# Kernel optimization log

Measured on AMD Instinct MI355X. Metric: run time of the kernel, lower is better.

Reference implementation:

```python
import jax, jax.numpy as jnp
import numpy as np

N = 8192
DIN = 256
DOUT = 128
ALPHA = 0.2      # leaky-relu negative slope
K_MAX = 32       # static upper bound on action.max()+1 (action in [0, 32))
NEG_BIG = -9.0e15


def setup_inputs() -> dict:
    key = jax.random.key(0)
    ks = jax.random.split(key, 6)
    xavier_w = 1.414 * np.sqrt(6.0 / (DIN + DOUT))
    xavier_a = 1.414 * np.sqrt(6.0 / (DOUT + 1))
    return {
        "input": jax.random.normal(ks[0], (N, DIN), dtype=jnp.float32),
        "adj": jax.random.randint(ks[1], (N, N), 0, 2, dtype=jnp.int32),
        "action": jax.random.randint(ks[2], (N,), 0, K_MAX, dtype=jnp.int32),
        "W": jax.random.uniform(ks[3], (DIN, DOUT), jnp.float32, -xavier_w, xavier_w),
        "a_self": jax.random.uniform(ks[4], (DOUT, 1), jnp.float32, -xavier_a, xavier_a),
        "a_neighs": jax.random.uniform(ks[5], (DOUT, 1), jnp.float32, -xavier_a, xavier_a),
        "breadth_policy": 1,
    }


def reference(input, adj, action, W, a_self, a_neighs, breadth_policy):
    h = input @ W                                  # [N, DOUT]
    attn_self = h @ a_self                         # [N, 1]
    attn_neighs = h @ a_neighs                     # [N, 1]
    e = jax.nn.leaky_relu(attn_self + attn_neighs.T, negative_slope=ALPHA)  # [N, N]
    masked = jnp.where(adj > 0, e, jnp.float32(NEG_BIG))
    attention = jax.nn.softmax(masked, axis=1)     # [N, N]
    if breadth_policy:
        # static K_MAX >= action.max()+1; thresholds only read index action[i]
        top_vals, _ = jax.lax.top_k(attention, K_MAX)          # [N, K_MAX], sorted desc
        thresholds = top_vals[jnp.arange(N), action]           # [N]
        attention = jnp.where(attention < thresholds[:, None], 0.0, attention)
    h_prime = attention @ h                        # [N, DOUT]
    return jax.nn.elu(h_prime)                     # concat=True
```

## Files before the change

kernel.cpp:

```cpp
#include <hip/hip_runtime.h>
#include <cstdint>
#include <cstddef>

#define NN   8192
#define DIN  256
#define DOUT 128
#define LRA  0.2f

__global__ __launch_bounds__(256) void gemm_h_kernel(
    const float* __restrict__ input, const float* __restrict__ W,
    float* __restrict__ h)
{
    __shared__ float tile[16][DIN];
    const int row0 = blockIdx.x * 16;
    {
        const float4* in4 = (const float4*)(input + (size_t)row0 * DIN);
        float4* t4 = (float4*)&tile[0][0];
        for (int k = threadIdx.x; k < 16 * DIN / 4; k += 256) t4[k] = in4[k];
    }
    __syncthreads();
    const int c = threadIdx.x & 127;
    const int g = threadIdx.x >> 7;
    float acc[8] = {0.f, 0.f, 0.f, 0.f, 0.f, 0.f, 0.f, 0.f};
    for (int k = 0; k < DIN; k += 4) {
        const float w0 = W[(k + 0) * DOUT + c];
        const float w1 = W[(k + 1) * DOUT + c];
        const float w2 = W[(k + 2) * DOUT + c];
        const float w3 = W[(k + 3) * DOUT + c];
        #pragma unroll
        for (int m = 0; m < 8; ++m) {
            const float4 av = *(const float4*)&tile[g * 8 + m][k];
            acc[m] += av.x * w0 + av.y * w1 + av.z * w2 + av.w * w3;
        }
    }
    #pragma unroll
    for (int m = 0; m < 8; ++m)
        h[(size_t)(row0 + g * 8 + m) * DOUT + c] = acc[m];
}

__global__ __launch_bounds__(256) void attn_vec_kernel(
    const float* __restrict__ h, const float* __restrict__ a_self,
    const float* __restrict__ a_neighs, float* __restrict__ s,
    float* __restrict__ t)
{
    const int wid  = (blockIdx.x * 256 + threadIdx.x) >> 6;
    const int lane = threadIdx.x & 63;
    if (wid >= NN) return;
    const float h0 = h[(size_t)wid * DOUT + lane];
    const float h1 = h[(size_t)wid * DOUT + 64 + lane];
    float vs = h0 * a_self[lane]   + h1 * a_self[64 + lane];
    float vn = h0 * a_neighs[lane] + h1 * a_neighs[64 + lane];
    for (int off = 32; off > 0; off >>= 1) {
        vs += __shfl_down(vs, off);
        vn += __shfl_down(vn, off);
    }
    if (lane == 0) { s[wid] = vs; t[wid] = vn; }
}

__global__ __launch_bounds__(256) void rank_kernel(
    const float* __restrict__ t, int* __restrict__ order)
{
    __shared__ float tl[NN];
    __shared__ int   part[8][32];
    for (int k = threadIdx.x; k < NN; k += 256) tl[k] = t[k];
    __syncthreads();
    const int jloc = threadIdx.x & 31;
    const int seg  = threadIdx.x >> 5;
    const int j    = blockIdx.x * 32 + jloc;
    const float tj = tl[j];
    int r = 0;
    const int k0 = seg * (NN / 8);
    for (int k = k0; k < k0 + NN / 8; ++k) {
        const float tk = tl[k];
        r += (tk > tj) ? 1 : ((tk == tj && k < j) ? 1 : 0);
    }
    part[seg][jloc] = r;
    __syncthreads();
    if (threadIdx.x < 32) {
        int rr = 0;
        #pragma unroll
        for (int ss = 0; ss < 8; ++ss) rr += part[ss][threadIdx.x];
        order[rr] = blockIdx.x * 32 + threadIdx.x;
    }
}

__global__ __launch_bounds__(256) void gat_row_kernel(
    const int* __restrict__ adj, const float* __restrict__ s_arr,
    const float* __restrict__ t_arr, const int* __restrict__ order,
    const int* __restrict__ action, const float* __restrict__ h,
    const int* __restrict__ policy, float* __restrict__ out)
{
    __shared__ float tl[NN];
    __shared__ float red[256];
    __shared__ float numlds[2][128];
    __shared__ int   sel_j[64];
    __shared__ float sel_w[64];
    __shared__ int   sel_cnt_sh;
    __shared__ int   done_sh;

    const int row = blockIdx.x;
    const int tid = threadIdx.x;
    {
        const float4* t4 = (const float4*)t_arr;
        float4* tl4 = (float4*)tl;
        for (int k = tid; k < NN / 4; k += 256) tl4[k] = t4[k];
    }
    __syncthreads();

    const float s    = s_arr[row];
    const float tmax = tl[order[0]];
    const float zc   = s + tmax;
    const float C    = fmaxf(zc, LRA * zc);

    const int4*   arow = (const int4*)(adj + (size_t)row * NN);
    const float4* tl4c = (const float4*)tl;
    float acc = 0.f;
    #pragma unroll
    for (int k = 0; k < 8; ++k) {
        const int idx = tid + k * 256;
        const int4   a  = arow[idx];
        const float4 tv = tl4c[idx];
        float z, e, w;
        z = s + tv.x; e = fmaxf(z, LRA * z); w = __expf(e - C); if (a.x > 0) acc += w;
        z = s + tv.y; e = fmaxf(z, LRA * z); w = __expf(e - C); if (a.y > 0) acc += w;
        z = s + tv.z; e = fmaxf(z, LRA * z); w = __expf(e - C); if (a.z > 0) acc += w;
        z = s + tv.w; e = fmaxf(z, LRA * z); w = __expf(e - C); if (a.w > 0) acc += w;
    }
    red[tid] = acc;
    __syncthreads();
    for (int off = 128; off > 0; off >>= 1) {
        if (tid < off) red[tid] += red[tid + off];
        __syncthreads();
    }
    const float l = red[0];

    int K = action[row] + 1;
    if (policy[0] == 0) K = 0x7FFFFFFF;
    const int c = tid & 127;
    const int g = tid >> 7;
    float accv = 0.f;

    const int lane = tid & 63;
    float tthr = -3.0e38f;
    int found = 0;
    int cnt = 0;
    int base = 0;

    while (true) {
        if (tid < 64) {
            const int p = base + lane;
            int j = 0, valid = 0;
            float tj = -3.0e38f;
            if (p < NN) {
                j     = order[p];
                tj    = tl[j];
                valid = (adj[(size_t)row * NN + j] > 0) ? 1 : 0;
            }
            const unsigned long long vm = __ballot(valid);
            if (!found) {
                const int cv = __popcll(vm);
                if (cnt + cv >= K) {
                    const int need = K - cnt;
                    const int myrank =
                        __popcll(vm & ((1ull << lane) - 1ull)) + 1;
                    const unsigned long long pm =
                        __ballot(valid && (myrank == need));
                    const int L = __ffsll((long long)pm) - 1;
                    tthr  = __shfl(tj, L);
                    found = 1;
                } else {
                    cnt += cv;
                }
            }
            const int selected = valid && (tj >= tthr);
            const unsigned long long sm = __ballot(selected);
            const int pos = __popcll(sm & ((1ull << lane) - 1ull));
            if (selected) {
                const float z = s + tj;
                const float e = fmaxf(z, LRA * z);
                sel_j[pos] = j;
                sel_w[pos] = __expf(e - C);
            }
            if (lane == 0) {
                sel_cnt_sh = __popcll(sm);
                const int nb = base + 64;
                int dn;
                if (nb >= NN)      dn = 1;
                else if (found)    dn = (tl[order[nb]] < tthr) ? 1 : 0;
                else               dn = 0;
                done_sh = dn;
            }
        }
        __syncthreads();
        const int nsel = sel_cnt_sh;
        const int dn   = done_sh;
        for (int e2 = g; e2 < nsel; e2 += 2)
            accv += sel_w[e2] * h[(size_t)sel_j[e2] * DOUT + c];
        base += 64;
        if (dn) break;
        __syncthreads();
    }

    numlds[g][c] = accv;
    __syncthreads();
    if (tid < 128) {
        const float v = (numlds[0][tid] + numlds[1][tid]) / l;
        out[(size_t)row * DOUT + tid] = (v > 0.f) ? v : expm1f(v);
    }
}

extern "C" void kernel_launch(void* const* d_in, const int* in_sizes, int n_in,
                              void* d_out, int out_size, void* d_ws,
                              size_t ws_size, hipStream_t stream)
{
    const float* input    = (const float*)d_in[0];
    const int*   adj      = (const int*)d_in[1];
    const int*   action   = (const int*)d_in[2];
    const float* W        = (const float*)d_in[3];
    const float* a_self   = (const float*)d_in[4];
    const float* a_neighs = (const float*)d_in[5];
    const int*   policy   = (const int*)d_in[6];
    float* out = (float*)d_out;

    float* ws    = (float*)d_ws;
    float* h     = ws;
    float* s     = ws + (size_t)NN * DOUT;
    float* t     = s + NN;
    int*   order = (int*)(t + NN);

    hipLaunchKernelGGL(gemm_h_kernel, dim3(512), dim3(256), 0, stream,
                       input, W, h);
    hipLaunchKernelGGL(attn_vec_kernel, dim3(2048), dim3(256), 0, stream,
                       h, a_self, a_neighs, s, t);
    hipLaunchKernelGGL(rank_kernel, dim3(256), dim3(256), 0, stream,
                       t, order);
    hipLaunchKernelGGL(gat_row_kernel, dim3(8192), dim3(256), 0, stream,
                       adj, s, t, order, action, h, policy, out);
}
```

Before: 429.8 us.

## Fuse all GAT stages into one cooperative persistent kernel with grid syncs

Replaces the four kernel launches (projection GEMM, attention vectors, ranking, per-row softmax/top-k aggregation) with one cooperative kernel of 512 blocks. Each block handles 16 rows end to end and uses grid.sync between phases. The attention-vector dot products are now computed straight from the GEMM accumulators. Ranking is redistributed so each block ranks its own 16 rows. The aim is to remove launch gaps and the reloads of t into LDS. The cost is only 512 blocks for the bandwidth-heavy adjacency phase (down from 8192), with each block looping over 16 rows serially, which may reduce latency hiding.

```diff
diff --git a/kernel.cpp b/kernel.cpp
--- a/kernel.cpp
+++ b/kernel.cpp
@@ -1,211 +1,227 @@
 #include <hip/hip_runtime.h>
+#include <hip/hip_cooperative_groups.h>
 #include <cstdint>
 #include <cstddef>
 
-#define NN   8192
-#define DIN  256
-#define DOUT 128
-#define LRA  0.2f
-
-__global__ __launch_bounds__(256) void gemm_h_kernel(
-    const float* __restrict__ input, const float* __restrict__ W,
-    float* __restrict__ h)
+namespace cg = cooperative_groups;
+
+#define NN    8192
+#define DIN   256
+#define DOUT  128
+#define LRA   0.2f
+#define RPB   16
+#define NB    512
+
+__global__ __launch_bounds__(256, 2) void gat_fused_kernel(
+    const float* __restrict__ input, const int* __restrict__ adj,
+    const int* __restrict__ action, const float* __restrict__ W,
+    const float* __restrict__ a_self, const float* __restrict__ a_neighs,
+    const int* __restrict__ policy, float* __restrict__ out,
+    float* __restrict__ h, float* __restrict__ s_arr,
+    float* __restrict__ t_arr, int* __restrict__ order)
 {
-    __shared__ float tile[16][DIN];
-    const int row0 = blockIdx.x * 16;
-    {
-        const float4* in4 = (const float4*)(input + (size_t)row0 * DIN);
-        float4* t4 = (float4*)&tile[0][0];
-        for (int k = threadIdx.x; k < 16 * DIN / 4; k += 256) t4[k] = in4[k];
-    }
-    __syncthreads();
-    const int c = threadIdx.x & 127;
-    const int g = threadIdx.x >> 7;
-    float acc[8] = {0.f, 0.f, 0.f, 0.f, 0.f, 0.f, 0.f, 0.f};
-    for (int k = 0; k < DIN; k += 4) {
-        const float w0 = W[(k + 0) * DOUT + c];
-        const float w1 = W[(k + 1) * DOUT + c];
-        const float w2 = W[(k + 2) * DOUT + c];
-        const float w3 = W[(k + 3) * DOUT + c];
-        #pragma unroll
-        for (int m = 0; m < 8; ++m) {
-            const float4 av = *(const float4*)&tile[g * 8 + m][k];
-            acc[m] += av.x * w0 + av.y * w1 + av.z * w2 + av.w * w3;
-        }
-    }
-    #pragma unroll
-    for (int m = 0; m < 8; ++m)
-        h[(size_t)(row0 + g * 8 + m) * DOUT + c] = acc[m];
-}
-
-__global__ __launch_bounds__(256) void attn_vec_kernel(
-    const float* __restrict__ h, const float* __restrict__ a_self,
-    const float* __restrict__ a_neighs, float* __restrict__ s,
-    float* __restrict__ t)
-{
-    const int wid  = (blockIdx.x * 256 + threadIdx.x) >> 6;
-    const int lane = threadIdx.x & 63;
-    if (wid >= NN) return;
-    const float h0 = h[(size_t)wid * DOUT + lane];
-    const float h1 = h[(size_t)wid * DOUT + 64 + lane];
-    float vs = h0 * a_self[lane]   + h1 * a_self[64 + lane];
-    float vn = h0 * a_neighs[lane] + h1 * a_neighs[64 + lane];
-    for (int off = 32; off > 0; off >>= 1) {
-        vs += __shfl_down(vs, off);
-        vn += __shfl_down(vn, off);
-    }
-    if (lane == 0) { s[wid] = vs; t[wid] = vn; }
-}
-
-__global__ __launch_bounds__(256) void rank_kernel(
-    const float* __restrict__ t, int* __restrict__ order)
-{
-    __shared__ float tl[NN];
-    __shared__ int   part[8][32];
-    for (int k = threadIdx.x; k < NN; k += 256) tl[k] = t[k];
-    __syncthreads();
-    const int jloc = threadIdx.x & 31;
-    const int seg  = threadIdx.x >> 5;
-    const int j    = blockIdx.x * 32 + jloc;
-    const float tj = tl[j];
-    int r = 0;
-    const int k0 = seg * (NN / 8);
-    for (int k = k0; k < k0 + NN / 8; ++k) {
-        const float tk = tl[k];
-        r += (tk > tj) ? 1 : ((tk == tj && k < j) ? 1 : 0);
-    }
-    part[seg][jloc] = r;
-    __syncthreads();
-    if (threadIdx.x < 32) {
-        int rr = 0;
-        #pragma unroll
-        for (int ss = 0; ss < 8; ++ss) rr += part[ss][threadIdx.x];
-        order[rr] = blockIdx.x * 32 + threadIdx.x;
-    }
-}
-
-__global__ __launch_bounds__(256) void gat_row_kernel(
-    const int* __restrict__ adj, const float* __restrict__ s_arr,
-    const float* __restrict__ t_arr, const int* __restrict__ order,
-    const int* __restrict__ action, const float* __restrict__ h,
-    const int* __restrict__ policy, float* __restrict__ out)
-{
-    __shared__ float tl[NN];
-    __shared__ float red[256];
-    __shared__ float numlds[2][128];
+    cg::grid_group grid = cg::this_grid();
+
+    __shared__ union {
+        float tile[RPB][DIN];
+        float tl[NN];
+    } u;
+    __shared__ float red[4];
+    __shared__ float numlds[2][DOUT];
+    __shared__ float pr[4][16];
+    __shared__ int   prank[4][RPB];
     __shared__ int   sel_j[64];
     __shared__ float sel_w[64];
     __shared__ int   sel_cnt_sh;
     __shared__ int   done_sh;
 
-    const int row = blockIdx.x;
-    const int tid = threadIdx.x;
+    const int tid  = threadIdx.x;
+    const int row0 = blockIdx.x * RPB;
+    const int c    = tid & 127;
+    const int g    = tid >> 7;
+    const int lane = tid & 63;
+    const int wave = tid >> 6;
+
+    {
+        const float4* in4 = (const float4*)(input + (size_t)row0 * DIN);
+        float4* t4 = (float4*)&u.tile[0][0];
+        #pragma unroll
+        for (int k = 0; k < 4; ++k) t4[tid + k * 256] = in4[tid + k * 256];
+    }
+    __syncthreads();
+    {
+        float acc[8];
+        #pragma unroll
+        for (int m = 0; m < 8; ++m) acc[m] = 0.f;
+        for (int k = 0; k < DIN; k += 4) {
+            const float w0 = W[(k + 0) * DOUT + c];
+            const float w1 = W[(k + 1) * DOUT + c];
+            const float w2 = W[(k + 2) * DOUT + c];
+            const float w3 = W[(k + 3) * DOUT + c];
+            #pragma unroll
+            for (int m = 0; m < 8; ++m) {
+                const float4 av = *(const float4*)&u.tile[g * 8 + m][k];
+                acc[m] += av.x * w0 + av.y * w1 + av.z * w2 + av.w * w3;
+            }
+        }
+        #pragma unroll
+        for (int m = 0; m < 8; ++m)
+            h[(size_t)(row0 + g * 8 + m) * DOUT + c] = acc[m];
+
+        const float as = a_self[c];
+        const float an = a_neighs[c];
+        #pragma unroll
+        for (int m = 0; m < 8; ++m) {
+            float vs = acc[m] * as;
+            float vt = acc[m] * an;
+            for (int off = 32; off > 0; off >>= 1) {
+                vs += __shfl_down(vs, off);
+                vt += __shfl_down(vt, off);
+            }
+            if (lane == 0) { pr[wave][2 * m] = vs; pr[wave][2 * m + 1] = vt; }
+        }
+    }
+    __syncthreads();
+    if (tid < 16) {
+        const int m  = tid & 7;
+        const int gg = tid >> 3;
+        const int r  = row0 + gg * 8 + m;
+        s_arr[r] = pr[2 * gg][2 * m]     + pr[2 * gg + 1][2 * m];
+        t_arr[r] = pr[2 * gg][2 * m + 1] + pr[2 * gg + 1][2 * m + 1];
+    }
+    grid.sync();
+
     {
         const float4* t4 = (const float4*)t_arr;
-        float4* tl4 = (float4*)tl;
-        for (int k = tid; k < NN / 4; k += 256) tl4[k] = t4[k];
+        float4* tl4 = (float4*)u.tl;
+        #pragma unroll
+        for (int k = 0; k < 8; ++k) tl4[tid + k * 256] = t4[tid + k * 256];
     }
     __syncthreads();
-
-    const float s    = s_arr[row];
-    const float tmax = tl[order[0]];
-    const float zc   = s + tmax;
-    const float C    = fmaxf(zc, LRA * zc);
-
-    const int4*   arow = (const int4*)(adj + (size_t)row * NN);
-    const float4* tl4c = (const float4*)tl;
-    float acc = 0.f;
-    #pragma unroll
-    for (int k = 0; k < 8; ++k) {
-        const int idx = tid + k * 256;
-        const int4   a  = arow[idx];
-        const float4 tv = tl4c[idx];
-        float z, e, w;
-        z = s + tv.x; e = fmaxf(z, LRA * z); w = __expf(e - C); if (a.x > 0) acc += w;
-        z = s + tv.y; e = fmaxf(z, LRA * z); w = __expf(e - C); if (a.y > 0) acc += w;
-        z = s + tv.z; e = fmaxf(z, LRA * z); w = __expf(e - C); if (a.z > 0) acc += w;
-        z = s + tv.w; e = fmaxf(z, LRA * z); w = __expf(e - C); if (a.w > 0) acc += w;
-    }
-    red[tid] = acc;
-    __syncthreads();
-    for (int off = 128; off > 0; off >>= 1) {
-        if (tid < off) red[tid] += red[tid + off];
-        __syncthreads();
-    }
-    const float l = red[0];
-
-    int K = action[row] + 1;
-    if (policy[0] == 0) K = 0x7FFFFFFF;
-    const int c = tid & 127;
-    const int g = tid >> 7;
-    float accv = 0.f;
-
-    const int lane = tid & 63;
-    float tthr = -3.0e38f;
-    int found = 0;
-    int cnt = 0;
-    int base = 0;
-
-    while (true) {
-        if (tid < 64) {
-            const int p = base + lane;
-            int j = 0, valid = 0;
-            float tj = -3.0e38f;
-            if (p < NN) {
-                j     = order[p];
-                tj    = tl[j];
-                valid = (adj[(size_t)row * NN + j] > 0) ? 1 : 0;
+    {
+        float tj[RPB];
+        int   r[RPB];
+        #pragma unroll
+        for (int q = 0; q < RPB; ++q) { tj[q] = u.tl[row0 + q]; r[q] = 0; }
+        const int kbase = tid * 32;
+        for (int it = 0; it < 32; ++it) {
+            const int k = kbase + ((it + tid) & 31);
+            const float tk = u.tl[k];
+            #pragma unroll
+            for (int q = 0; q < RPB; ++q)
+                r[q] += (tk > tj[q] || (tk == tj[q] && k < row0 + q)) ? 1 : 0;
+        }
+        #pragma unroll
+        for (int q = 0; q < RPB; ++q) {
+            int v = r[q];
+            for (int off = 32; off > 0; off >>= 1) v += __shfl_down(v, off);
+            if (lane == 0) prank[wave][q] = v;
+        }
+        __syncthreads();
+        if (tid < RPB) {
+            const int rr = prank[0][tid] + prank[1][tid] +
+                           prank[2][tid] + prank[3][tid];
+            order[rr] = row0 + tid;
+        }
+    }
+    grid.sync();
+
+    const int policyv = policy[0];
+    const float tmax  = u.tl[order[0]];
+    const float4* tl4c = (const float4*)u.tl;
+
+    for (int rr = 0; rr < RPB; ++rr) {
+        const int row = row0 + rr;
+        const float s  = s_arr[row];
+        const float zc = s + tmax;
+        const float C  = fmaxf(zc, LRA * zc);
+
+        const int4* arow = (const int4*)(adj + (size_t)row * NN);
+        float acc = 0.f;
+        #pragma unroll
+        for (int k = 0; k < 8; ++k) {
+            const int idx = tid + k * 256;
+            const int4   a  = arow[idx];
+            const float4 tv = tl4c[idx];
+            float z, e;
+            z = s + tv.x; e = fmaxf(z, LRA * z); if (a.x > 0) acc += __expf(e - C);
+            z = s + tv.y; e = fmaxf(z, LRA * z); if (a.y > 0) acc += __expf(e - C);
+            z = s + tv.z; e = fmaxf(z, LRA * z); if (a.z > 0) acc += __expf(e - C);
+            z = s + tv.w; e = fmaxf(z, LRA * z); if (a.w > 0) acc += __expf(e - C);
+        }
+        for (int off = 32; off > 0; off >>= 1) acc += __shfl_down(acc, off);
+        if (lane == 0) red[wave] = acc;
+        __syncthreads();
+        const float l = red[0] + red[1] + red[2] + red[3];
+
+        int K = action[row] + 1;
+        if (policyv == 0) K = 0x7FFFFFFF;
+        float accv = 0.f;
+        float tthr = -3.0e38f;
+        int found = 0, cnt = 0, base = 0;
+
+        while (true) {
+            if (tid < 64) {
+                const int p = base + lane;
+                int j = 0, valid = 0;
+                float tjv = -3.0e38f;
+                if (p < NN) {
+                    j     = order[p];
+                    tjv   = u.tl[j];
+                    valid = (adj[(size_t)row * NN + j] > 0) ? 1 : 0;
+                }
+                const unsigned long long vm = __ballot(valid);
+                if (!found) {
+                    const int cv = __popcll(vm);
+                    if (cnt + cv >= K) {
+                        const int need = K - cnt;
+                        const int myrank =
+                            __popcll(vm & ((1ull << lane) - 1ull)) + 1;
+                        const unsigned long long pm =
+                            __ballot(valid && (myrank == need));
+                        const int L = __ffsll((long long)pm) - 1;
+                        tthr  = __shfl(tjv, L);
+                        found = 1;
+                    } else {
+                        cnt += cv;
+                    }
+                }
+                const int selected = valid && (tjv >= tthr);
+                const unsigned long long sm = __ballot(selected);
+                const int pos = __popcll(sm & ((1ull << lane) - 1ull));
+                if (selected) {
+                    const float z = s + tjv;
+                    const float e = fmaxf(z, LRA * z);
+                    sel_j[pos] = j;
+                    sel_w[pos] = __expf(e - C);
+                }
+                if (lane == 0) {
+                    sel_cnt_sh = __popcll(sm);
+                    const int nb = base + 64;
+                    int dn;
+                    if (nb >= NN)   dn = 1;
+                    else if (found) dn = (u.tl[order[nb]] < tthr) ? 1 : 0;
+                    else            dn = 0;
+                    done_sh = dn;
+                }
             }
-            const unsigned long long vm = __ballot(valid);
-            if (!found) {
-                const int cv = __popcll(vm);
-                if (cnt + cv >= K) {
-                    const int need = K - cnt;
-                    const int myrank =
-                        __popcll(vm & ((1ull << lane) - 1ull)) + 1;
-                    const unsigned long long pm =
-                        __ballot(valid && (myrank == need));
-                    const int L = __ffsll((long long)pm) - 1;
-                    tthr  = __shfl(tj, L);
-                    found = 1;
-                } else {
-                    cnt += cv;
-                }
-            }
-            const int selected = valid && (tj >= tthr);
-            const unsigned long long sm = __ballot(selected);
-            const int pos = __popcll(sm & ((1ull << lane) - 1ull));
-            if (selected) {
-                const float z = s + tj;
-                const float e = fmaxf(z, LRA * z);
-                sel_j[pos] = j;
-                sel_w[pos] = __expf(e - C);
-            }
-            if (lane == 0) {
-                sel_cnt_sh = __popcll(sm);
-                const int nb = base + 64;
-                int dn;
-                if (nb >= NN)      dn = 1;
-                else if (found)    dn = (tl[order[nb]] < tthr) ? 1 : 0;
-                else               dn = 0;
-                done_sh = dn;
-            }
-        }
-        __syncthreads();
-        const int nsel = sel_cnt_sh;
-        const int dn   = done_sh;
-        for (int e2 = g; e2 < nsel; e2 += 2)
-            accv += sel_w[e2] * h[(size_t)sel_j[e2] * DOUT + c];
-        base += 64;
-        if (dn) break;
-        __syncthreads();
-    }
-
-    numlds[g][c] = accv;
-    __syncthreads();
-    if (tid < 128) {
-        const float v = (numlds[0][tid] + numlds[1][tid]) / l;
-        out[(size_t)row * DOUT + tid] = (v > 0.f) ? v : expm1f(v);
+            __syncthreads();
+            const int nsel = sel_cnt_sh;
+            const int dn   = done_sh;
+            for (int e2 = g; e2 < nsel; e2 += 2)
+                accv += sel_w[e2] * h[(size_t)sel_j[e2] * DOUT + c];
+            base += 64;
+            if (dn) break;
+            __syncthreads();
+        }
+
+        numlds[g][c] = accv;
+        __syncthreads();
+        if (tid < 128) {
+            const float v = (numlds[0][tid] + numlds[1][tid]) / l;
+            out[(size_t)row * DOUT + tid] = (v > 0.f) ? v : expm1f(v);
+        }
+        __syncthreads();
     }
 }
 
@@ -228,12 +244,10 @@
     float* t     = s + NN;
     int*   order = (int*)(t + NN);
 
-    hipLaunchKernelGGL(gemm_h_kernel, dim3(512), dim3(256), 0, stream,
-                       input, W, h);
-    hipLaunchKernelGGL(attn_vec_kernel, dim3(2048), dim3(256), 0, stream,
-                       h, a_self, a_neighs, s, t);
-    hipLaunchKernelGGL(rank_kernel, dim3(256), dim3(256), 0, stream,
-                       t, order);
-    hipLaunchKernelGGL(gat_row_kernel, dim3(8192), dim3(256), 0, stream,
-                       adj, s, t, order, action, h, policy, out);
+    void* args[] = { (void*)&input, (void*)&adj, (void*)&action, (void*)&W,
+                     (void*)&a_self, (void*)&a_neighs, (void*)&policy,
+                     (void*)&out, (void*)&h, (void*)&s, (void*)&t,
+                     (void*)&order };
+    hipLaunchCooperativeKernel((const void*)gat_fused_kernel, dim3(NB),
+                               dim3(256), args, 0, stream);
 }
```

After: 547.9 us. +27.5%, slower.
